# Optimization experiments

Measured on AMD Instinct MI355X. Metric: run time of the kernel, lower is better.

Reference implementation:

```python
import jax, jax.numpy as jnp
import numpy as np

B, L, D, H, E, K = 16, 197, 768, 12, 8, 2
HID = 4 * D
HD = D // H
SCALE = HD ** -0.5
EPS = 1e-5


def _layernorm(x, g, b):
    m = jnp.mean(x, axis=-1, keepdims=True)
    v = jnp.mean((x - m) ** 2, axis=-1, keepdims=True)
    return (x - m) * jax.lax.rsqrt(v + EPS) * g + b


def setup_inputs() -> dict:
    key = jax.random.key(0)
    ks = jax.random.split(key, 8)
    s = 0.02
    return {
        "x": jax.random.normal(ks[0], (B, L, D), jnp.float32),
        "ln1_g": jnp.ones((D,), jnp.float32),
        "ln1_b": jnp.zeros((D,), jnp.float32),
        "qkv_w": jax.random.normal(ks[1], (D, 3 * D), jnp.float32) * s,
        "qkv_b": jnp.zeros((3 * D,), jnp.float32),
        "proj_w": jax.random.normal(ks[2], (D, D), jnp.float32) * s,
        "proj_b": jnp.zeros((D,), jnp.float32),
        "ln2_g": jnp.ones((D,), jnp.float32),
        "ln2_b": jnp.zeros((D,), jnp.float32),
        "w_gate": jax.random.normal(ks[3], (D, E), jnp.float32) * s,
        "w1": jax.random.normal(ks[4], (E, D, HID), jnp.float32) * s,
        "b1": jnp.zeros((E, HID), jnp.float32),
        "w2": jax.random.normal(ks[5], (E, HID, D), jnp.float32) * s,
        "b2": jnp.zeros((E, D), jnp.float32),
    }


def reference(x, ln1_g, ln1_b, qkv_w, qkv_b, proj_w, proj_b,
              ln2_g, ln2_b, w_gate, w1, b1, w2, b2):
    # --- attention branch: x = x + attn(norm1(x)) ---
    h = _layernorm(x, ln1_g, ln1_b)
    qkv = (h @ qkv_w + qkv_b).reshape(B, L, 3, H, HD)
    q, k, v = [qkv[:, :, i].transpose(0, 2, 1, 3) for i in range(3)]  # [B,H,L,HD]
    attn = jax.nn.softmax(jnp.einsum('bhqd,bhkd->bhqk', q, k) * SCALE, axis=-1)
    o = jnp.einsum('bhqk,bhkd->bhqd', attn, v).transpose(0, 2, 1, 3).reshape(B, L, D)
    x = x + o @ proj_w + proj_b

    # --- MoE FFN branch on norm2(x), tokens flattened ---
    flat = _layernorm(x, ln2_g, ln2_b).reshape(-1, D)  # [T, D], T = B*L
    T = flat.shape[0]
    # noisy top-k gating, eval path (no noise): top-(k+1) logits, softmax over top-k
    logits = flat @ w_gate                              # [T, E]
    top_vals, top_idx = jax.lax.top_k(logits, K + 1)
    probs = jax.nn.softmax(top_vals[:, :K], axis=-1)    # [T, K]
    gates = jnp.zeros((T, E), flat.dtype).at[
        jnp.arange(T)[:, None], top_idx[:, :K]].set(probs)  # sparse gate matrix

    # dense equivalent of SparseDispatcher dispatch -> expert MLP -> combine:
    # output[t] = sum_e gates[t,e] * (gelu(flat @ w1[e] + b1[e]) @ w2[e] + b2[e])
    hid = jax.nn.gelu(jnp.einsum('td,edf->tef', flat, w1) + b1, approximate=False)
    y = jnp.einsum('te,tef,efd->td', gates, hid, w2) + gates @ b2
    return x + y.reshape(B, L, D)
```

## Files before the change

### kernel.cpp

```cpp
#include <hip/hip_runtime.h>
#include <math.h>
#include <stdint.h>

typedef unsigned short u16;
typedef unsigned int u32;
typedef float floatx4 __attribute__((ext_vector_type(4)));
typedef __bf16 bf16x8 __attribute__((ext_vector_type(8)));

#define T_TOK 3152
#define SEQ 197
#define NH 12
#define LISTN 7424
#define MOE_MT 58
#define YHALF ((size_t)LISTN * 768)

__device__ __forceinline__ float bf2f(u16 u) { return __uint_as_float(((u32)u) << 16); }
__device__ __forceinline__ u16 f2bf(float f) {
    u32 u = __float_as_uint(f);
    u += 0x7FFFu + ((u >> 16) & 1u);
    return (u16)(u >> 16);
}
__device__ __forceinline__ float wred_sum(float v) {
#pragma unroll
    for (int off = 32; off; off >>= 1) v += __shfl_xor(v, off);
    return v;
}

__device__ __forceinline__ float gelu_fast(float v) {
    float x = fabsf(v) * 0.70710678118654752f;
    float t = __builtin_amdgcn_rcpf(fmaf(0.3275911f, x, 1.0f));
    float p = t * fmaf(t, fmaf(t, fmaf(t, fmaf(t, 1.061405429f, -1.453152027f),
                                       1.421413741f), -0.284496736f), 0.254829592f);
    float er = fmaf(-p, __expf(-x * x), 1.0f);
    er = copysignf(er, v);
    return 0.5f * v * (1.0f + er);
}

#define GLB_AS(p) ((const __attribute__((address_space(1))) void*)(uintptr_t)(p))
#define LDS_AS(p) ((__attribute__((address_space(3))) void*)(uintptr_t)(p))
__device__ __forceinline__ void gl_lds16(const u16* g, u16* l) {
    __builtin_amdgcn_global_load_lds(GLB_AS(g), LDS_AS(l), 16, 0, 0);
}

template <int SPLIT>
__global__ __launch_bounds__(256) void transp_kernel(const float* __restrict__ in,
        u16* __restrict__ oh, u16* __restrict__ ol, int R, int C) {
    int r0 = blockIdx.x * 64, c0 = blockIdx.y * 64;
    size_t zo = (size_t)blockIdx.z * R * C;
    __shared__ float Lt[64][68];
    int tid = threadIdx.x;
    int rr = tid >> 2, cs = (tid & 3) * 16;
    const float* src = in + zo + (size_t)(r0 + rr) * C + c0 + cs;
#pragma unroll
    for (int i = 0; i < 4; i++) *(float4*)&Lt[rr][cs + i * 4] = *(const float4*)(src + i * 4);
    __syncthreads();
    int cw = tid >> 2, rs = (tid & 3) * 16;
    u16 hv[16], lv[16];
#pragma unroll
    for (int j = 0; j < 16; j++) {
        float v = Lt[rs + j][cw];
        u16 hb = f2bf(v);
        hv[j] = hb;
        if (SPLIT) lv[j] = f2bf(v - bf2f(hb));
    }
    u16* dst = oh + zo + (size_t)(c0 + cw) * R + r0 + rs;
    *(uint4*)dst = *(const uint4*)&hv[0];
    *(uint4*)(dst + 8) = *(const uint4*)&hv[8];
    if (SPLIT) {
        u16* dstl = ol + zo + (size_t)(c0 + cw) * R + r0 + rs;
        *(uint4*)dstl = *(const uint4*)&lv[0];
        *(uint4*)(dstl + 8) = *(const uint4*)&lv[8];
    }
}

__global__ __launch_bounds__(256) void ln1_kernel(const float* __restrict__ x,
        const float* __restrict__ g, const float* __restrict__ b,
        u16* __restrict__ h_hi, u16* __restrict__ h_lo) {
    int t = blockIdx.x, tid = threadIdx.x;
    int w = tid >> 6, lane = tid & 63;
    float v[3];
#pragma unroll
    for (int i = 0; i < 3; i++) v[i] = x[(size_t)t * 768 + tid + i * 256];
    float s = v[0] + v[1] + v[2];
    float q = v[0] * v[0] + v[1] * v[1] + v[2] * v[2];
    s = wred_sum(s); q = wred_sum(q);
    __shared__ float red[8];
    if (lane == 0) { red[w] = s; red[4 + w] = q; }
    __syncthreads();
    float st = red[0] + red[1] + red[2] + red[3];
    float qt = red[4] + red[5] + red[6] + red[7];
    float mean = st * (1.f / 768.f);
    float var = qt * (1.f / 768.f) - mean * mean;
    float rs = rsqrtf(var + 1e-5f);
#pragma unroll
    for (int i = 0; i < 3; i++) {
        int d = tid + i * 256;
        float hv = (v[i] - mean) * rs * g[d] + b[d];
        u16 hi = f2bf(hv);
        h_hi[(size_t)t * 768 + d] = hi;
        h_lo[(size_t)t * 768 + d] = f2bf(hv - bf2f(hi));
    }
}

template <int MODE>
__global__ __launch_bounds__(256) void gemm128(const u16* __restrict__ Ah,
        const u16* __restrict__ Al, const u16* __restrict__ Bh, const u16* __restrict__ Bl,
        const float* __restrict__ bias, void* __restrict__ Cv, void* __restrict__ Cv2,
        const float* __restrict__ resid,
        const int* __restrict__ list, const int* __restrict__ asg, int M, int N, int K) {
    constexpr bool SPLIT = (MODE <= 1);
    constexpr int GX = (MODE <= 1) ? 25 : MOE_MT;
    constexpr int GY = (MODE == 0) ? 18 : (MODE == 2) ? 24 : 6;
    constexpr int GZ = (MODE == 3) ? 2 : 1;
    constexpr int G  = GX * GY * GZ;
    constexpr int NT = GY * GZ;
    constexpr int Q8 = G >> 3, R8 = G & 7;

    int d = blockIdx.x + GX * (blockIdx.y + GY * blockIdx.z);
    int j = d & 7, s = d >> 3;
    int v = (j < R8) ? (j * (Q8 + 1) + s) : (R8 * (Q8 + 1) + (j - R8) * Q8 + s);
    int mt = v / NT, nzr = v - mt * NT;
    int yt = nzr % GY, zt = nzr / GY;
    int m0 = mt * 128, n0 = yt * 128;

    const u16* Bph = Bh;
    const float* bp = bias;
    const u16* Bpl = Bl;
    if (MODE >= 2) {
        if (m0 >= asg[8]) return;
        int e = 0;
        while (m0 >= asg[e + 1]) ++e;
        Bph = Bh + (size_t)e * N * K;
        bp = bias + (size_t)e * N;
    }
    int kbeg = 0, kend = K;
    if (MODE == 3) { int kh = K >> 1; kbeg = zt * kh; kend = kbeg + kh; }

    __shared__ __align__(16) u16 SM[32768];
    u16* Ash = SM;
    u16* Bsh = SM + (SPLIT ? 8192 : 16384);
    u16* Asl = SM + 16384;
    u16* Bsl = SM + 24576;

    int tid = threadIdx.x;
    int w = tid >> 6, lane = tid & 63, l15 = lane & 15, quad = lane >> 4;
    int wm = (w & 1) * 64, wn = (w >> 1) * 64;
    int lr = lane >> 2;
    int lc = ((lane & 3) ^ ((lane >> 3) & 3)) * 8;

    const u16* ga[2]; const u16* gal[2];
    const u16* gb[2]; const u16* gbl[2];
    int ldro[2];
#pragma unroll
    for (int it = 0; it < 2; it++) {
        int arow = m0 + it * 64 + w * 16 + lr;
        if (MODE == 2) {
            int entry = list[arow];
            ga[it] = Ah + (size_t)(entry >= 0 ? (entry >> 1) : 0) * K + lc;
        } else if (MODE == 3) {
            ga[it] = Ah + (size_t)arow * K + lc;
        } else {
            int rc = min(arow, M - 1);
            ga[it] = Ah + (size_t)rc * K + lc;
            gal[it] = Al + (size_t)rc * K + lc;
        }
        int brow = n0 + it * 64 + w * 16 + lr;
        gb[it] = Bph + (size_t)brow * K + lc;
        if (SPLIT) gbl[it] = Bpl + (size_t)brow * K + lc;
        ldro[it] = (it * 64 + w * 16) * 32;
    }

    int ra[4], rb[4];
#pragma unroll
    for (int i = 0; i < 4; i++) {
        int r1 = wm + i * 16 + l15;
        ra[i] = r1 * 32 + (quad ^ ((r1 >> 1) & 3)) * 8;
        int r2 = wn + i * 16 + l15;
        rb[i] = r2 * 32 + (quad ^ ((r2 >> 1) & 3)) * 8;
    }

    floatx4 acc[4][4];
#pragma unroll
    for (int mi = 0; mi < 4; mi++)
#pragma unroll
        for (int ni = 0; ni < 4; ni++) acc[mi][ni] = (floatx4){0.f, 0.f, 0.f, 0.f};

    auto stage = [&](int buf, int k0) {
        int bo = buf * 4096;
#pragma unroll
        for (int it = 0; it < 2; it++) {
            gl_lds16(ga[it] + k0, &Ash[bo + ldro[it]]);
            gl_lds16(gb[it] + k0, &Bsh[bo + ldro[it]]);
            if constexpr (SPLIT) {
                gl_lds16(gal[it] + k0, &Asl[bo + ldro[it]]);
                gl_lds16(gbl[it] + k0, &Bsl[bo + ldro[it]]);
            }
        }
    };
    auto compute = [&](int buf) {
        int bo = buf * 4096;
        bf16x8 afh[4], bfh[4], afl[4], bfl[4];
#pragma unroll
        for (int i = 0; i < 4; i++) {
            afh[i] = *(const bf16x8*)&Ash[bo + ra[i]];
            bfh[i] = *(const bf16x8*)&Bsh[bo + rb[i]];
            if constexpr (SPLIT) {
                afl[i] = *(const bf16x8*)&Asl[bo + ra[i]];
                bfl[i] = *(const bf16x8*)&Bsl[bo + rb[i]];
            }
        }
        if constexpr (!SPLIT) __builtin_amdgcn_s_setprio(1);
#pragma unroll
        for (int mi = 0; mi < 4; mi++)
#pragma unroll
            for (int ni = 0; ni < 4; ni++) {
                if constexpr (SPLIT) {
                    acc[mi][ni] = __builtin_amdgcn_mfma_f32_16x16x32_bf16(afl[mi], bfh[ni], acc[mi][ni], 0, 0, 0);
                    acc[mi][ni] = __builtin_amdgcn_mfma_f32_16x16x32_bf16(afh[mi], bfl[ni], acc[mi][ni], 0, 0, 0);
                }
                acc[mi][ni] = __builtin_amdgcn_mfma_f32_16x16x32_bf16(afh[mi], bfh[ni], acc[mi][ni], 0, 0, 0);
            }
        if constexpr (!SPLIT) __builtin_amdgcn_s_setprio(0);
    };

    int nsteps = (kend - kbeg) >> 5;
    if constexpr (SPLIT) {
        stage(0, kbeg);
        __syncthreads();
        for (int s2 = 0; s2 < nsteps; s2 += 2) {
            int k0 = kbeg + s2 * 32;
            stage(1, k0 + 32);
            compute(0);
            __syncthreads();
            if (s2 + 2 < nsteps) stage(0, k0 + 64);
            compute(1);
            __syncthreads();
        }
    } else {
        stage(0, kbeg);
        stage(1, kbeg + 32);
        stage(2, kbeg + 64);
        asm volatile("s_waitcnt vmcnt(8)" ::: "memory");
        __builtin_amdgcn_s_barrier();
        for (int t = 0; t < nsteps; ++t) {
            if (t + 3 < nsteps) stage((t + 3) & 3, kbeg + (t + 3) * 32);
            compute(t & 3);
            if (t + 3 < nsteps) {
                asm volatile("s_waitcnt vmcnt(8) lgkmcnt(0)" ::: "memory");
            } else if (t + 2 < nsteps) {
                asm volatile("s_waitcnt vmcnt(4) lgkmcnt(0)" ::: "memory");
            } else {
                asm volatile("s_waitcnt vmcnt(0) lgkmcnt(0)" ::: "memory");
            }
            __builtin_amdgcn_s_barrier();
        }
    }

    if constexpr (MODE == 2) {
#pragma unroll
        for (int ni = 0; ni < 4; ni++) {
            int col = wn + ni * 16 + l15;
            float bb = bp[n0 + col];
#pragma unroll
            for (int mi = 0; mi < 4; mi++) {
#pragma unroll
                for (int r = 0; r < 4; r++) {
                    int row = wm + mi * 16 + quad * 4 + r;
                    float gv = gelu_fast(acc[mi][ni][r] + bb);
                    SM[row * 128 + (col ^ ((row & 7) << 3))] = f2bf(gv);
                }
            }
        }
        __syncthreads();
        int rr = tid >> 1, half = (tid & 1) * 64;
        int grow = m0 + rr;
        if (list[grow] >= 0) {
            u16* dst = (u16*)Cv + (size_t)grow * N + n0 + half;
            int xr = (rr & 7) << 3;
#pragma unroll
            for (int gch = 0; gch < 8; gch++) {
                int cb = (half + gch * 8) ^ xr;
                *(uint4*)(dst + gch * 8) = *(const uint4*)&SM[rr * 128 + cb];
            }
        }
        return;
    }

    float* Cf = (float*)Cv;
    if (MODE == 3) Cf += (size_t)zt * ((size_t)M * N);
#pragma unroll
    for (int ni = 0; ni < 4; ni++) {
        int col = n0 + wn + ni * 16 + l15;
        float bb = bp[col];
        if (MODE == 3 && zt != 0) bb = 0.f;
#pragma unroll
        for (int mi = 0; mi < 4; mi++) {
#pragma unroll
            for (int r = 0; r < 4; r++) {
                int row = m0 + wm + mi * 16 + quad * 4 + r;
                float v2 = acc[mi][ni][r] + bb;
                if (MODE == 0) {
                    if (row < M) {
                        u16 hb = f2bf(v2);
                        ((u16*)Cv)[(size_t)row * N + col] = hb;
                        ((u16*)Cv2)[(size_t)row * N + col] = f2bf(v2 - bf2f(hb));
                    }
                } else if (MODE == 1) {
                    if (row < M) Cf[(size_t)row * N + col] = v2 + resid[(size_t)row * N + col];
                } else {
                    if (list[row] >= 0) Cf[(size_t)row * N + col] = v2;
                }
            }
        }
    }
}

__global__ __launch_bounds__(256) void attn_mfma_kernel(const u16* __restrict__ qph,
        const u16* __restrict__ qpl, u16* __restrict__ ohi, u16* __restrict__ olo) {
    int d = blockIdx.x + 4 * blockIdx.y;
    int j = d & 7, sdx = d >> 3;
    int v = j * 96 + sdx;
    int qbase = (v & 3) * 64;
    int by = v >> 2;
    int b = by / NH, h = by % NH;
    int tid = threadIdx.x;
    int w = tid >> 6, lane = tid & 63, l15 = lane & 15, quad = lane >> 4;

    __shared__ u16 Qh[64 * 64], Ql[64 * 64];
    __shared__ u16 Sh[64 * 64], Sl[64 * 64];
    __shared__ u16 Ph[64 * 72], Pl[64 * 72];

    int grow8 = lane >> 3;
    int gsrc = ((lane & 7) ^ grow8) * 8;
    int srow = tid >> 2;
    int scol = (tid & 3) * 16;

#pragma unroll
    for (int it = 0; it < 2; it++) {
        int r = qbase + w * 16 + it * 8 + grow8;
        int rc = min(r, SEQ - 1);
        size_t so = (size_t)(b * SEQ + rc) * 2304 + h * 64 + gsrc;
        gl_lds16(qph + so, &Qh[(w * 16 + it * 8) * 64]);
        gl_lds16(qpl + so, &Ql[(w * 16 + it * 8) * 64]);
    }
    __syncthreads();
    bf16x8 aqh[2], aql[2];
#pragma unroll
    for (int s2 = 0; s2 < 2; s2++) {
        int row = w * 16 + l15;
        int ad = row * 64 + (((s2 * 4 + quad) ^ (row & 7))) * 8;
        aqh[s2] = *(const bf16x8*)&Qh[ad];
        aql[s2] = *(const bf16x8*)&Ql[ad];
    }

    floatx4 sc[16];
#pragma unroll
    for (int f = 0; f < 16; f++) sc[f] = (floatx4){0.f, 0.f, 0.f, 0.f};

    for (int t = 0; t < 4; t++) {
#pragma unroll
        for (int it = 0; it < 2; it++) {
            int r = t * 64 + w * 16 + it * 8 + grow8;
            int rc = min(r, SEQ - 1);
            size_t so = (size_t)(b * SEQ + rc) * 2304 + 768 + h * 64 + gsrc;
            gl_lds16(qph + so, &Sh[(w * 16 + it * 8) * 64]);
            gl_lds16(qpl + so, &Sl[(w * 16 + it * 8) * 64]);
        }
        __syncthreads();
#pragma unroll
        for (int s = 0; s < 4; s++) {
            int row = s * 16 + l15;
#pragma unroll
            for (int s2 = 0; s2 < 2; s2++) {
                int ad = row * 64 + (((s2 * 4 + quad) ^ (row & 7))) * 8;
                bf16x8 bkh = *(const bf16x8*)&Sh[ad];
                bf16x8 bkl = *(const bf16x8*)&Sl[ad];
                sc[t * 4 + s] = __builtin_amdgcn_mfma_f32_16x16x32_bf16(aql[s2], bkh, sc[t * 4 + s], 0, 0, 0);
                sc[t * 4 + s] = __builtin_amdgcn_mfma_f32_16x16x32_bf16(aqh[s2], bkl, sc[t * 4 + s], 0, 0, 0);
                sc[t * 4 + s] = __builtin_amdgcn_mfma_f32_16x16x32_bf16(aqh[s2], bkh, sc[t * 4 + s], 0, 0, 0);
            }
        }
        __syncthreads();
    }

    float m[4] = {-1e30f, -1e30f, -1e30f, -1e30f};
#pragma unroll
    for (int f = 0; f < 16; f++) {
        int key = (f >> 2) * 64 + (f & 3) * 16 + l15;
        bool valid = key < SEQ;
#pragma unroll
        for (int r = 0; r < 4; r++) {
            float s = valid ? sc[f][r] * 0.125f : -1e30f;
            sc[f][r] = s;
            m[r] = fmaxf(m[r], s);
        }
    }
#pragma unroll
    for (int r = 0; r < 4; r++) {
#pragma unroll
        for (int off = 1; off < 16; off <<= 1) m[r] = fmaxf(m[r], __shfl_xor(m[r], off));
    }
    float sum[4] = {0.f, 0.f, 0.f, 0.f};
#pragma unroll
    for (int f = 0; f < 16; f++) {
#pragma unroll
        for (int r = 0; r < 4; r++) {
            float p = expf(sc[f][r] - m[r]);
            sc[f][r] = p;
            sum[r] += p;
        }
    }
    float inv[4];
#pragma unroll
    for (int r = 0; r < 4; r++) {
#pragma unroll
        for (int off = 1; off < 16; off <<= 1) sum[r] += __shfl_xor(sum[r], off);
        inv[r] = 1.f / sum[r];
    }

    floatx4 oacc[4];
#pragma unroll
    for (int sd = 0; sd < 4; sd++) oacc[sd] = (floatx4){0.f, 0.f, 0.f, 0.f};

    for (int t = 0; t < 4; t++) {
#pragma unroll
        for (int s = 0; s < 4; s++) {
#pragma unroll
            for (int r = 0; r < 4; r++) {
                float p = sc[t * 4 + s][r];
                u16 hb = f2bf(p);
                int row = w * 16 + quad * 4 + r;
                Ph[row * 72 + s * 16 + l15] = hb;
                Pl[row * 72 + s * 16 + l15] = f2bf(p - bf2f(hb));
            }
        }
        {
            int key = t * 64 + srow;
            int kc = min(key, SEQ - 1);
            size_t so = (size_t)(b * SEQ + kc) * 2304 + 1536 + h * 64 + scol;
            u16 hv[16], lv[16];
            *(uint4*)&hv[0] = *(const uint4*)(qph + so);
            *(uint4*)&hv[8] = *(const uint4*)(qph + so + 8);
            *(uint4*)&lv[0] = *(const uint4*)(qpl + so);
            *(uint4*)&lv[8] = *(const uint4*)(qpl + so + 8);
            int kg = srow >> 3, kw = srow & 7;
#pragma unroll
            for (int i = 0; i < 16; i++) {
                int dcol = scol + i;
                int idx = dcol * 64 + ((kg ^ (dcol & 7)) * 8) + kw;
                Sh[idx] = hv[i];
                Sl[idx] = lv[i];
            }
        }
        __syncthreads();
#pragma unroll
        for (int s2 = 0; s2 < 2; s2++) {
            bf16x8 aph = *(const bf16x8*)&Ph[(w * 16 + l15) * 72 + s2 * 32 + quad * 8];
            bf16x8 apl = *(const bf16x8*)&Pl[(w * 16 + l15) * 72 + s2 * 32 + quad * 8];
#pragma unroll
            for (int sd = 0; sd < 4; sd++) {
                int row = sd * 16 + l15;
                int ad = row * 64 + (((s2 * 4 + quad) ^ (row & 7))) * 8;
                bf16x8 bvh = *(const bf16x8*)&Sh[ad];
                bf16x8 bvl = *(const bf16x8*)&Sl[ad];
                oacc[sd] = __builtin_amdgcn_mfma_f32_16x16x32_bf16(apl, bvh, oacc[sd], 0, 0, 0);
                oacc[sd] = __builtin_amdgcn_mfma_f32_16x16x32_bf16(aph, bvl, oacc[sd], 0, 0, 0);
                oacc[sd] = __builtin_amdgcn_mfma_f32_16x16x32_bf16(aph, bvh, oacc[sd], 0, 0, 0);
            }
        }
        __syncthreads();
    }

#pragma unroll
    for (int sd = 0; sd < 4; sd++) {
#pragma unroll
        for (int r = 0; r < 4; r++) {
            int q = qbase + w * 16 + quad * 4 + r;
            if (q < SEQ) {
                float val = oacc[sd][r] * inv[r];
                u16 hb = f2bf(val);
                size_t o = ((size_t)(b * SEQ + q)) * 768 + h * 64 + sd * 16 + l15;
                ohi[o] = hb;
                olo[o] = f2bf(val - bf2f(hb));
            }
        }
    }
}

__global__ __launch_bounds__(256) void ln2_gate_kernel(const float* __restrict__ x1,
        const float* __restrict__ g, const float* __restrict__ b, const float* __restrict__ wg,
        u16* __restrict__ flat, int2* __restrict__ idx, float2* __restrict__ gate) {
    int t = blockIdx.x, tid = threadIdx.x;
    int w = tid >> 6, lane = tid & 63;
    float v[3];
#pragma unroll
    for (int i = 0; i < 3; i++) v[i] = x1[(size_t)t * 768 + tid + i * 256];
    float s = v[0] + v[1] + v[2];
    float q = v[0] * v[0] + v[1] * v[1] + v[2] * v[2];
    s = wred_sum(s); q = wred_sum(q);
    __shared__ float red[8];
    __shared__ float fs[768];
    __shared__ float lg[8];
    if (lane == 0) { red[w] = s; red[4 + w] = q; }
    __syncthreads();
    float st = red[0] + red[1] + red[2] + red[3];
    float qt = red[4] + red[5] + red[6] + red[7];
    float mean = st * (1.f / 768.f);
    float var = qt * (1.f / 768.f) - mean * mean;
    float rs = rsqrtf(var + 1e-5f);
#pragma unroll
    for (int i = 0; i < 3; i++) {
        int d = tid + i * 256;
        float f = (v[i] - mean) * rs * g[d] + b[d];
        flat[(size_t)t * 768 + d] = f2bf(f);
        fs[d] = f;
    }
    __syncthreads();
    int e0 = 2 * w, e1 = 2 * w + 1;
    float p0 = 0.f, p1 = 0.f;
    for (int d = lane; d < 768; d += 64) {
        float f = fs[d];
        p0 += f * wg[d * 8 + e0];
        p1 += f * wg[d * 8 + e1];
    }
    p0 = wred_sum(p0); p1 = wred_sum(p1);
    if (lane == 0) { lg[e0] = p0; lg[e1] = p1; }
    __syncthreads();
    if (tid == 0) {
        float b0 = -1e30f, b1 = -1e30f;
        int i0 = 0, i1 = 0;
        for (int e = 0; e < 8; e++) {
            float le = lg[e];
            if (le > b0) { b1 = b0; i1 = i0; b0 = le; i0 = e; }
            else if (le > b1) { b1 = le; i1 = e; }
        }
        float ex = expf(b1 - b0);
        float den = 1.f + ex;
        idx[t] = make_int2(i0, i1);
        gate[t] = make_float2(1.f / den, ex / den);
    }
}

__global__ __launch_bounds__(256) void hist_kernel(const int2* __restrict__ idx, int* __restrict__ cnt) {
    int t = blockIdx.x * 256 + threadIdx.x;
    if (t < T_TOK) {
        int2 id = idx[t];
        atomicAdd(&cnt[id.x], 1);
        atomicAdd(&cnt[id.y], 1);
    }
}

__global__ void offsets_kernel(const int* __restrict__ cnt, int* __restrict__ asg) {
    if (threadIdx.x == 0 && blockIdx.x == 0) {
        int acc = 0;
        asg[0] = 0;
        for (int e = 0; e < 8; e++) { acc += (cnt[e] + 127) & ~127; asg[e + 1] = acc; }
    }
}

__global__ __launch_bounds__(256) void scatter_kernel(const int2* __restrict__ idx,
        const int* __restrict__ asg, int* __restrict__ cursor,
        int* __restrict__ list, int* __restrict__ pos) {
    int t = blockIdx.x * 256 + threadIdx.x;
    if (t >= T_TOK) return;
    int2 id = idx[t];
    int p0 = asg[id.x] + atomicAdd(&cursor[id.x], 1);
    list[p0] = t * 2;
    pos[t * 2] = p0;
    int p1 = asg[id.y] + atomicAdd(&cursor[id.y], 1);
    list[p1] = t * 2 + 1;
    pos[t * 2 + 1] = p1;
}

__global__ __launch_bounds__(256) void final_kernel(const float* __restrict__ x1,
        const float* __restrict__ yp, const int* __restrict__ pos,
        const float2* __restrict__ gate, float* __restrict__ out) {
    int t = blockIdx.x, tid = threadIdx.x;
    float2 g = gate[t];
    int p0 = pos[t * 2], p1 = pos[t * 2 + 1];
#pragma unroll
    for (int i = 0; i < 3; i++) {
        int d = tid + i * 256;
        float y0 = yp[(size_t)p0 * 768 + d] + yp[YHALF + (size_t)p0 * 768 + d];
        float y1 = yp[(size_t)p1 * 768 + d] + yp[YHALF + (size_t)p1 * 768 + d];
        out[(size_t)t * 768 + d] = x1[(size_t)t * 768 + d] + g.x * y0 + g.y * y1;
    }
}

extern "C" void kernel_launch(void* const* d_in, const int* in_sizes, int n_in,
                              void* d_out, int out_size, void* d_ws, size_t ws_size,
                              hipStream_t stream) {
    const float* x      = (const float*)d_in[0];
    const float* ln1_g  = (const float*)d_in[1];
    const float* ln1_b  = (const float*)d_in[2];
    const float* qkv_w  = (const float*)d_in[3];
    const float* qkv_b  = (const float*)d_in[4];
    const float* proj_w = (const float*)d_in[5];
    const float* proj_b = (const float*)d_in[6];
    const float* ln2_g  = (const float*)d_in[7];
    const float* ln2_b  = (const float*)d_in[8];
    const float* w_gate = (const float*)d_in[9];
    const float* w1     = (const float*)d_in[10];
    const float* b1     = (const float*)d_in[11];
    const float* w2     = (const float*)d_in[12];
    const float* b2     = (const float*)d_in[13];

    char* ws = (char*)d_ws;
    size_t off = 0;
    auto alloc = [&](size_t bytes) { size_t cur = off; off = (off + bytes + 255) & ~(size_t)255; return cur; };
    u16*    h_hi   = (u16*)   (ws + alloc((size_t)T_TOK * 768 * 2));
    u16*    h_lo   = (u16*)   (ws + alloc((size_t)T_TOK * 768 * 2));
    u16*    qkv_hi = (u16*)   (ws + alloc((size_t)T_TOK * 2304 * 2));
    u16*    qkv_lo = (u16*)   (ws + alloc((size_t)T_TOK * 2304 * 2));
    u16*    o_hi   = (u16*)   (ws + alloc((size_t)T_TOK * 768 * 2));
    u16*    o_lo   = (u16*)   (ws + alloc((size_t)T_TOK * 768 * 2));
    float*  ypair  = (float*) ws;
    float*  x1     = (float*) (ws + alloc((size_t)T_TOK * 768 * 4));
    u16*    flat   = (u16*)   (ws + alloc((size_t)T_TOK * 768 * 2));
    int2*   idx    = (int2*)  (ws + alloc((size_t)T_TOK * 8));
    float2* gate   = (float2*)(ws + alloc((size_t)T_TOK * 8));
    int*    cnt    = (int*)   (ws + alloc(64));
    int*    cursor = cnt + 8;
    int*    asg    = (int*)   (ws + alloc(64));
    int*    list   = (int*)   (ws + alloc((size_t)LISTN * 4));
    int*    pos    = (int*)   (ws + alloc((size_t)T_TOK * 2 * 4));
    u16*    hid    = (u16*)   (ws + alloc((size_t)LISTN * 3072 * 2));
    u16*    qkvt_h = (u16*)   (ws + alloc((size_t)2304 * 768 * 2));
    u16*    qkvt_l = (u16*)   (ws + alloc((size_t)2304 * 768 * 2));
    u16*    projt_h = (u16*)  (ws + alloc((size_t)768 * 768 * 2));
    u16*    projt_l = (u16*)  (ws + alloc((size_t)768 * 768 * 2));
    u16*    w1t    = (u16*)   (ws + alloc((size_t)8 * 3072 * 768 * 2));
    u16*    w2t    = (u16*)   (ws + alloc((size_t)8 * 768 * 3072 * 2));

    hipMemsetAsync(cnt, 0, 64, stream);
    hipMemsetAsync(list, 0xFF, (size_t)LISTN * 4, stream);

    transp_kernel<1><<<dim3(12, 36, 1), 256, 0, stream>>>(qkv_w, qkvt_h, qkvt_l, 768, 2304);
    transp_kernel<1><<<dim3(12, 12, 1), 256, 0, stream>>>(proj_w, projt_h, projt_l, 768, 768);
    transp_kernel<0><<<dim3(12, 48, 8), 256, 0, stream>>>(w1, w1t, nullptr, 768, 3072);
    transp_kernel<0><<<dim3(48, 12, 8), 256, 0, stream>>>(w2, w2t, nullptr, 3072, 768);

    ln1_kernel<<<T_TOK, 256, 0, stream>>>(x, ln1_g, ln1_b, h_hi, h_lo);
    gemm128<0><<<dim3(25, 18), 256, 0, stream>>>(h_hi, h_lo, qkvt_h, qkvt_l, qkv_b, qkv_hi,
                                                 qkv_lo, nullptr, nullptr, nullptr, T_TOK, 2304, 768);
    attn_mfma_kernel<<<dim3(4, 192), 256, 0, stream>>>(qkv_hi, qkv_lo, o_hi, o_lo);
    gemm128<1><<<dim3(25, 6), 256, 0, stream>>>(o_hi, o_lo, projt_h, projt_l, proj_b, x1,
                                                nullptr, x, nullptr, nullptr, T_TOK, 768, 768);
    ln2_gate_kernel<<<T_TOK, 256, 0, stream>>>(x1, ln2_g, ln2_b, w_gate, flat, idx, gate);
    hist_kernel<<<(T_TOK + 255) / 256, 256, 0, stream>>>(idx, cnt);
    offsets_kernel<<<1, 64, 0, stream>>>(cnt, asg);
    scatter_kernel<<<(T_TOK + 255) / 256, 256, 0, stream>>>(idx, asg, cursor, list, pos);
    gemm128<2><<<dim3(MOE_MT, 24), 256, 0, stream>>>(flat, nullptr, w1t, nullptr, b1, hid,
                                                     nullptr, nullptr, list, asg, LISTN, 3072, 768);
    gemm128<3><<<dim3(MOE_MT, 6, 2), 256, 0, stream>>>(hid, nullptr, w2t, nullptr, b2, ypair,
                                                       nullptr, nullptr, list, asg, LISTN, 768, 3072);
    final_kernel<<<T_TOK, 256, 0, stream>>>(x1, ypair, pos, gate, (float*)d_out);
}
```

Before: 536.8 us.

## Use a 256x256-tile 512-thread kernel for the MoE first GEMM

Replaces the 128x128 MODE-2 expert up-projection GEMM with a dedicated 256x256-tile kernel. It runs eight waves, double-buffers LDS and fuses gathered-row loads with the bias+GELU epilogue. The goal is more data reuse per loaded tile and fewer weight re-reads. To match the tile, expert segments are padded to 256 rows, which enlarges the list and adds some padding work. The down-projection GEMM drops from a 4-stage to a 3-stage LDS pipeline to cut shared memory, and its second split-K partial is written into the dead w1t buffer.

Measured after the change: 653.9 us. +21.8%, slower.

```diff
diff --git a/kernel.cpp b/kernel.cpp
--- a/kernel.cpp
+++ b/kernel.cpp
@@ -10,9 +10,9 @@
 #define T_TOK 3152
 #define SEQ 197
 #define NH 12
-#define LISTN 7424
-#define MOE_MT 58
-#define YHALF ((size_t)LISTN * 768)
+#define LISTN 8448
+#define MOE1_MT 33
+#define MOE2_MT 66
 
 __device__ __forceinline__ float bf2f(u16 u) { return __uint_as_float(((u32)u) << 16); }
 __device__ __forceinline__ u16 f2bf(float f) {
@@ -109,8 +109,8 @@
         const float* __restrict__ resid,
         const int* __restrict__ list, const int* __restrict__ asg, int M, int N, int K) {
     constexpr bool SPLIT = (MODE <= 1);
-    constexpr int GX = (MODE <= 1) ? 25 : MOE_MT;
-    constexpr int GY = (MODE == 0) ? 18 : (MODE == 2) ? 24 : 6;
+    constexpr int GX = (MODE <= 1) ? 25 : MOE2_MT;
+    constexpr int GY = (MODE == 0) ? 18 : 6;
     constexpr int GZ = (MODE == 3) ? 2 : 1;
     constexpr int G  = GX * GY * GZ;
     constexpr int NT = GY * GZ;
@@ -126,7 +126,7 @@
     const u16* Bph = Bh;
     const float* bp = bias;
     const u16* Bpl = Bl;
-    if (MODE >= 2) {
+    if (MODE == 3) {
         if (m0 >= asg[8]) return;
         int e = 0;
         while (m0 >= asg[e + 1]) ++e;
@@ -136,9 +136,9 @@
     int kbeg = 0, kend = K;
     if (MODE == 3) { int kh = K >> 1; kbeg = zt * kh; kend = kbeg + kh; }
 
-    __shared__ __align__(16) u16 SM[32768];
+    __shared__ __align__(16) u16 SM[SPLIT ? 32768 : 24576];
     u16* Ash = SM;
-    u16* Bsh = SM + (SPLIT ? 8192 : 16384);
+    u16* Bsh = SM + (SPLIT ? 8192 : 12288);
     u16* Asl = SM + 16384;
     u16* Bsl = SM + 24576;
 
@@ -154,10 +154,7 @@
 #pragma unroll
     for (int it = 0; it < 2; it++) {
         int arow = m0 + it * 64 + w * 16 + lr;
-        if (MODE == 2) {
-            int entry = list[arow];
-            ga[it] = Ah + (size_t)(entry >= 0 ? (entry >> 1) : 0) * K + lc;
-        } else if (MODE == 3) {
+        if (MODE == 3) {
             ga[it] = Ah + (size_t)arow * K + lc;
         } else {
             int rc = min(arow, M - 1);
@@ -239,55 +236,25 @@
     } else {
         stage(0, kbeg);
         stage(1, kbeg + 32);
-        stage(2, kbeg + 64);
-        asm volatile("s_waitcnt vmcnt(8)" ::: "memory");
+        asm volatile("s_waitcnt vmcnt(4)" ::: "memory");
         __builtin_amdgcn_s_barrier();
+        int bufc = 0;
         for (int t = 0; t < nsteps; ++t) {
-            if (t + 3 < nsteps) stage((t + 3) & 3, kbeg + (t + 3) * 32);
-            compute(t & 3);
-            if (t + 3 < nsteps) {
-                asm volatile("s_waitcnt vmcnt(8) lgkmcnt(0)" ::: "memory");
-            } else if (t + 2 < nsteps) {
+            int b2 = bufc + 2; if (b2 >= 3) b2 -= 3;
+            if (t + 2 < nsteps) stage(b2, kbeg + (t + 2) * 32);
+            compute(bufc);
+            if (t + 2 < nsteps) {
                 asm volatile("s_waitcnt vmcnt(4) lgkmcnt(0)" ::: "memory");
             } else {
                 asm volatile("s_waitcnt vmcnt(0) lgkmcnt(0)" ::: "memory");
             }
             __builtin_amdgcn_s_barrier();
-        }
-    }
-
-    if constexpr (MODE == 2) {
-#pragma unroll
-        for (int ni = 0; ni < 4; ni++) {
-            int col = wn + ni * 16 + l15;
-            float bb = bp[n0 + col];
-#pragma unroll
-            for (int mi = 0; mi < 4; mi++) {
-#pragma unroll
-                for (int r = 0; r < 4; r++) {
-                    int row = wm + mi * 16 + quad * 4 + r;
-                    float gv = gelu_fast(acc[mi][ni][r] + bb);
-                    SM[row * 128 + (col ^ ((row & 7) << 3))] = f2bf(gv);
-                }
-            }
-        }
-        __syncthreads();
-        int rr = tid >> 1, half = (tid & 1) * 64;
-        int grow = m0 + rr;
-        if (list[grow] >= 0) {
-            u16* dst = (u16*)Cv + (size_t)grow * N + n0 + half;
-            int xr = (rr & 7) << 3;
-#pragma unroll
-            for (int gch = 0; gch < 8; gch++) {
-                int cb = (half + gch * 8) ^ xr;
-                *(uint4*)(dst + gch * 8) = *(const uint4*)&SM[rr * 128 + cb];
-            }
-        }
-        return;
+            bufc = (bufc == 2) ? 0 : bufc + 1;
+        }
     }
 
     float* Cf = (float*)Cv;
-    if (MODE == 3) Cf += (size_t)zt * ((size_t)M * N);
+    if (MODE == 3 && zt != 0) Cf = (float*)Cv2;
 #pragma unroll
     for (int ni = 0; ni < 4; ni++) {
         int col = n0 + wn + ni * 16 + l15;
@@ -315,6 +282,122 @@
     }
 }
 
+__global__ __launch_bounds__(512, 1) void gemm256_moe1(const u16* __restrict__ Ah,
+        const u16* __restrict__ Bh, const float* __restrict__ bias, u16* __restrict__ Cv,
+        const int* __restrict__ list, const int* __restrict__ asg) {
+    constexpr int GX = MOE1_MT, GY = 12, G = GX * GY;
+    constexpr int Q8 = G >> 3, R8 = G & 7;
+    constexpr int N = 3072, K = 768, NSTEP = 24;
+
+    int d = blockIdx.x + GX * blockIdx.y;
+    int j = d & 7, s = d >> 3;
+    int v = (j < R8) ? (j * (Q8 + 1) + s) : (R8 * (Q8 + 1) + (j - R8) * Q8 + s);
+    int mt = v / GY, yt = v - mt * GY;
+    int m0 = mt * 256, n0 = yt * 256;
+    if (m0 >= asg[8]) return;
+    int e = 0;
+    while (m0 >= asg[e + 1]) ++e;
+    const u16* Bph = Bh + (size_t)e * N * K;
+    const float* bp = bias + (size_t)e * N;
+
+    __shared__ __align__(16) u16 SM[32768];
+
+    int tid = threadIdx.x;
+    int w = tid >> 6, lane = tid & 63, l15 = lane & 15, quad = lane >> 4;
+    int wr = w >> 2, wc = w & 3;
+    int lc = ((lane & 3) ^ ((lane >> 3) & 3)) * 8;
+
+    int ar0 = m0 + (tid >> 2);
+    int le0 = list[ar0], le1 = list[ar0 + 128];
+    const u16* gA0 = Ah + (size_t)(le0 >= 0 ? (le0 >> 1) : 0) * K + lc;
+    const u16* gA1 = Ah + (size_t)(le1 >= 0 ? (le1 >> 1) : 0) * K + lc;
+    const u16* gB0 = Bph + (size_t)(n0 + (tid >> 2)) * K + lc;
+    const u16* gB1 = Bph + (size_t)(n0 + 128 + (tid >> 2)) * K + lc;
+    int chunk = w * 512;
+
+    int ra[8], rb[4];
+#pragma unroll
+    for (int i = 0; i < 8; i++) { int r = wr * 128 + i * 16 + l15; ra[i] = r * 32 + (quad ^ ((r >> 1) & 3)) * 8; }
+#pragma unroll
+    for (int i = 0; i < 4; i++) { int r = wc * 64 + i * 16 + l15; rb[i] = r * 32 + (quad ^ ((r >> 1) & 3)) * 8; }
+
+    floatx4 acc[8][4];
+#pragma unroll
+    for (int i = 0; i < 8; i++)
+#pragma unroll
+        for (int j2 = 0; j2 < 4; j2++) acc[i][j2] = (floatx4){0.f, 0.f, 0.f, 0.f};
+
+    auto stage = [&](int buf, int k0) {
+        u16* la = &SM[buf * 8192];
+        u16* lb = &SM[16384 + buf * 8192];
+        gl_lds16(gA0 + k0, la + chunk);
+        gl_lds16(gA1 + k0, la + 4096 + chunk);
+        gl_lds16(gB0 + k0, lb + chunk);
+        gl_lds16(gB1 + k0, lb + 4096 + chunk);
+    };
+    auto compute = [&](int buf) {
+        const u16* la = &SM[buf * 8192];
+        const u16* lb = &SM[16384 + buf * 8192];
+        bf16x8 af[8], bf[4];
+#pragma unroll
+        for (int i = 0; i < 8; i++) af[i] = *(const bf16x8*)&la[ra[i]];
+#pragma unroll
+        for (int i = 0; i < 4; i++) bf[i] = *(const bf16x8*)&lb[rb[i]];
+        __builtin_amdgcn_s_setprio(1);
+#pragma unroll
+        for (int i = 0; i < 8; i++)
+#pragma unroll
+            for (int j2 = 0; j2 < 4; j2++)
+                acc[i][j2] = __builtin_amdgcn_mfma_f32_16x16x32_bf16(af[i], bf[j2], acc[i][j2], 0, 0, 0);
+        __builtin_amdgcn_s_setprio(0);
+    };
+
+    stage(0, 0);
+    for (int t = 0; t < NSTEP; ++t) {
+        if (t + 1 < NSTEP) {
+            stage((t + 1) & 1, (t + 1) * 32);
+            asm volatile("s_waitcnt vmcnt(4)" ::: "memory");
+        } else {
+            asm volatile("s_waitcnt vmcnt(0)" ::: "memory");
+        }
+        __builtin_amdgcn_s_barrier();
+        compute(t & 1);
+        __builtin_amdgcn_s_barrier();
+    }
+
+#pragma unroll
+    for (int p = 0; p < 2; p++) {
+        if (wr == p) {
+#pragma unroll
+            for (int j2 = 0; j2 < 4; j2++) {
+                int col = wc * 64 + j2 * 16 + l15;
+                float bb = bp[n0 + col];
+#pragma unroll
+                for (int i = 0; i < 8; i++) {
+#pragma unroll
+                    for (int r = 0; r < 4; r++) {
+                        int row = i * 16 + quad * 4 + r;
+                        SM[row * 256 + (col ^ ((row & 7) << 3))] = f2bf(gelu_fast(acc[i][j2][r] + bb));
+                    }
+                }
+            }
+        }
+        __syncthreads();
+        int row = tid >> 2, cb0 = (tid & 3) * 64;
+        int grow = m0 + p * 128 + row;
+        if (list[grow] >= 0) {
+            u16* dst = Cv + (size_t)grow * N + n0 + cb0;
+            int xr = (row & 7) << 3;
+#pragma unroll
+            for (int ch = 0; ch < 8; ch++) {
+                int cc = (cb0 + ch * 8) ^ xr;
+                *(uint4*)(dst + ch * 8) = *(const uint4*)&SM[row * 256 + cc];
+            }
+        }
+        __syncthreads();
+    }
+}
+
 __global__ __launch_bounds__(256) void attn_mfma_kernel(const u16* __restrict__ qph,
         const u16* __restrict__ qpl, u16* __restrict__ ohi, u16* __restrict__ olo) {
     int d = blockIdx.x + 4 * blockIdx.y;
@@ -554,7 +637,7 @@
     if (threadIdx.x == 0 && blockIdx.x == 0) {
         int acc = 0;
         asg[0] = 0;
-        for (int e = 0; e < 8; e++) { acc += (cnt[e] + 127) & ~127; asg[e + 1] = acc; }
+        for (int e = 0; e < 8; e++) { acc += (cnt[e] + 255) & ~255; asg[e + 1] = acc; }
     }
 }
 
@@ -573,7 +656,7 @@
 }
 
 __global__ __launch_bounds__(256) void final_kernel(const float* __restrict__ x1,
-        const float* __restrict__ yp, const int* __restrict__ pos,
+        const float* __restrict__ yp0, const float* __restrict__ yp1, const int* __restrict__ pos,
         const float2* __restrict__ gate, float* __restrict__ out) {
     int t = blockIdx.x, tid = threadIdx.x;
     float2 g = gate[t];
@@ -581,8 +664,8 @@
 #pragma unroll
     for (int i = 0; i < 3; i++) {
         int d = tid + i * 256;
-        float y0 = yp[(size_t)p0 * 768 + d] + yp[YHALF + (size_t)p0 * 768 + d];
-        float y1 = yp[(size_t)p1 * 768 + d] + yp[YHALF + (size_t)p1 * 768 + d];
+        float y0 = yp0[(size_t)p0 * 768 + d] + yp1[(size_t)p0 * 768 + d];
+        float y1 = yp0[(size_t)p1 * 768 + d] + yp1[(size_t)p1 * 768 + d];
         out[(size_t)t * 768 + d] = x1[(size_t)t * 768 + d] + g.x * y0 + g.y * y1;
     }
 }
@@ -614,7 +697,7 @@
     u16*    qkv_lo = (u16*)   (ws + alloc((size_t)T_TOK * 2304 * 2));
     u16*    o_hi   = (u16*)   (ws + alloc((size_t)T_TOK * 768 * 2));
     u16*    o_lo   = (u16*)   (ws + alloc((size_t)T_TOK * 768 * 2));
-    float*  ypair  = (float*) ws;
+    float*  ypair0 = (float*) ws;
     float*  x1     = (float*) (ws + alloc((size_t)T_TOK * 768 * 4));
     u16*    flat   = (u16*)   (ws + alloc((size_t)T_TOK * 768 * 2));
     int2*   idx    = (int2*)  (ws + alloc((size_t)T_TOK * 8));
@@ -631,6 +714,7 @@
     u16*    projt_l = (u16*)  (ws + alloc((size_t)768 * 768 * 2));
     u16*    w1t    = (u16*)   (ws + alloc((size_t)8 * 3072 * 768 * 2));
     u16*    w2t    = (u16*)   (ws + alloc((size_t)8 * 768 * 3072 * 2));
+    float*  ypair1 = (float*) w1t;
 
     hipMemsetAsync(cnt, 0, 64, stream);
     hipMemsetAsync(list, 0xFF, (size_t)LISTN * 4, stream);
@@ -650,9 +734,8 @@
     hist_kernel<<<(T_TOK + 255) / 256, 256, 0, stream>>>(idx, cnt);
     offsets_kernel<<<1, 64, 0, stream>>>(cnt, asg);
     scatter_kernel<<<(T_TOK + 255) / 256, 256, 0, stream>>>(idx, asg, cursor, list, pos);
-    gemm128<2><<<dim3(MOE_MT, 24), 256, 0, stream>>>(flat, nullptr, w1t, nullptr, b1, hid,
-                                                     nullptr, nullptr, list, asg, LISTN, 3072, 768);
-    gemm128<3><<<dim3(MOE_MT, 6, 2), 256, 0, stream>>>(hid, nullptr, w2t, nullptr, b2, ypair,
-                                                       nullptr, nullptr, list, asg, LISTN, 768, 3072);
-    final_kernel<<<T_TOK, 256, 0, stream>>>(x1, ypair, pos, gate, (float*)d_out);
-}
+    gemm256_moe1<<<dim3(MOE1_MT, 12), 512, 0, stream>>>(flat, w1t, b1, hid, list, asg);
+    gemm128<3><<<dim3(MOE2_MT, 6, 2), 256, 0, stream>>>(hid, nullptr, w2t, nullptr, b2, ypair0,
+                                                        ypair1, nullptr, list, asg, LISTN, 768, 3072);
+    final_kernel<<<T_TOK, 256, 0, stream>>>(x1, ypair0, ypair1, pos, gate, (float*)d_out);
+}
```

## Rework GEMM LDS pipelining and fuse expert histogram into gating kernel

Applied to the files above, without the earlier changes.

The SPLIT GEMM path switches from a double buffer with full __syncthreads to explicit vmcnt waits and raw barriers, and it now raises wave priority around the MFMA block. The non-split path goes from four to three LDS stages, which shrinks shared memory to allow more resident blocks at the cost of a shallower prefetch. The expert-count histogram moves into ln2_gate_kernel as atomics, removing one kernel launch. The second split-K partial buffer is relocated into the w1t region, which is dead by the time the second expert GEMM runs.

Result: slower. 583.7 us (+8.7%).

```diff
diff --git a/kernel.cpp b/kernel.cpp
--- a/kernel.cpp
+++ b/kernel.cpp
@@ -12,7 +12,6 @@
 #define NH 12
 #define LISTN 7424
 #define MOE_MT 58
-#define YHALF ((size_t)LISTN * 768)
 
 __device__ __forceinline__ float bf2f(u16 u) { return __uint_as_float(((u32)u) << 16); }
 __device__ __forceinline__ u16 f2bf(float f) {
@@ -136,9 +135,9 @@
     int kbeg = 0, kend = K;
     if (MODE == 3) { int kh = K >> 1; kbeg = zt * kh; kend = kbeg + kh; }
 
-    __shared__ __align__(16) u16 SM[32768];
+    __shared__ __align__(16) u16 SM[SPLIT ? 32768 : 24576];
     u16* Ash = SM;
-    u16* Bsh = SM + (SPLIT ? 8192 : 16384);
+    u16* Bsh = SM + (SPLIT ? 8192 : 12288);
     u16* Asl = SM + 16384;
     u16* Bsl = SM + 24576;
 
@@ -209,7 +208,7 @@
                 bfl[i] = *(const bf16x8*)&Bsl[bo + rb[i]];
             }
         }
-        if constexpr (!SPLIT) __builtin_amdgcn_s_setprio(1);
+        __builtin_amdgcn_s_setprio(1);
 #pragma unroll
         for (int mi = 0; mi < 4; mi++)
 #pragma unroll
@@ -220,39 +219,43 @@
                 }
                 acc[mi][ni] = __builtin_amdgcn_mfma_f32_16x16x32_bf16(afh[mi], bfh[ni], acc[mi][ni], 0, 0, 0);
             }
-        if constexpr (!SPLIT) __builtin_amdgcn_s_setprio(0);
+        __builtin_amdgcn_s_setprio(0);
     };
 
     int nsteps = (kend - kbeg) >> 5;
     if constexpr (SPLIT) {
         stage(0, kbeg);
-        __syncthreads();
-        for (int s2 = 0; s2 < nsteps; s2 += 2) {
-            int k0 = kbeg + s2 * 32;
-            stage(1, k0 + 32);
-            compute(0);
-            __syncthreads();
-            if (s2 + 2 < nsteps) stage(0, k0 + 64);
-            compute(1);
-            __syncthreads();
+        stage(1, kbeg + 32);
+        asm volatile("s_waitcnt vmcnt(8)" ::: "memory");
+        __builtin_amdgcn_s_barrier();
+        for (int t = 0; t < nsteps; ++t) {
+            compute(t & 1);
+            asm volatile("s_waitcnt lgkmcnt(0)" ::: "memory");
+            __builtin_amdgcn_s_barrier();
+            if (t + 2 < nsteps) {
+                stage(t & 1, kbeg + (t + 2) * 32);
+                asm volatile("s_waitcnt vmcnt(8)" ::: "memory");
+            } else if (t + 1 < nsteps) {
+                asm volatile("s_waitcnt vmcnt(0)" ::: "memory");
+            }
         }
     } else {
         stage(0, kbeg);
         stage(1, kbeg + 32);
-        stage(2, kbeg + 64);
-        asm volatile("s_waitcnt vmcnt(8)" ::: "memory");
+        asm volatile("s_waitcnt vmcnt(4)" ::: "memory");
         __builtin_amdgcn_s_barrier();
+        int bufc = 0;
         for (int t = 0; t < nsteps; ++t) {
-            if (t + 3 < nsteps) stage((t + 3) & 3, kbeg + (t + 3) * 32);
-            compute(t & 3);
-            if (t + 3 < nsteps) {
-                asm volatile("s_waitcnt vmcnt(8) lgkmcnt(0)" ::: "memory");
-            } else if (t + 2 < nsteps) {
+            int b2 = bufc + 2; if (b2 >= 3) b2 -= 3;
+            if (t + 2 < nsteps) stage(b2, kbeg + (t + 2) * 32);
+            compute(bufc);
+            if (t + 2 < nsteps) {
                 asm volatile("s_waitcnt vmcnt(4) lgkmcnt(0)" ::: "memory");
             } else {
                 asm volatile("s_waitcnt vmcnt(0) lgkmcnt(0)" ::: "memory");
             }
             __builtin_amdgcn_s_barrier();
+            bufc = (bufc == 2) ? 0 : bufc + 1;
         }
     }
 
@@ -287,7 +290,7 @@
     }
 
     float* Cf = (float*)Cv;
-    if (MODE == 3) Cf += (size_t)zt * ((size_t)M * N);
+    if (MODE == 3 && zt != 0) Cf = (float*)Cv2;
 #pragma unroll
     for (int ni = 0; ni < 4; ni++) {
         int col = n0 + wn + ni * 16 + l15;
@@ -489,7 +492,8 @@
 
 __global__ __launch_bounds__(256) void ln2_gate_kernel(const float* __restrict__ x1,
         const float* __restrict__ g, const float* __restrict__ b, const float* __restrict__ wg,
-        u16* __restrict__ flat, int2* __restrict__ idx, float2* __restrict__ gate) {
+        u16* __restrict__ flat, int2* __restrict__ idx, float2* __restrict__ gate,
+        int* __restrict__ cnt) {
     int t = blockIdx.x, tid = threadIdx.x;
     int w = tid >> 6, lane = tid & 63;
     float v[3];
@@ -538,15 +542,8 @@
         float den = 1.f + ex;
         idx[t] = make_int2(i0, i1);
         gate[t] = make_float2(1.f / den, ex / den);
-    }
-}
-
-__global__ __launch_bounds__(256) void hist_kernel(const int2* __restrict__ idx, int* __restrict__ cnt) {
-    int t = blockIdx.x * 256 + threadIdx.x;
-    if (t < T_TOK) {
-        int2 id = idx[t];
-        atomicAdd(&cnt[id.x], 1);
-        atomicAdd(&cnt[id.y], 1);
+        atomicAdd(&cnt[i0], 1);
+        atomicAdd(&cnt[i1], 1);
     }
 }
 
@@ -573,7 +570,7 @@
 }
 
 __global__ __launch_bounds__(256) void final_kernel(const float* __restrict__ x1,
-        const float* __restrict__ yp, const int* __restrict__ pos,
+        const float* __restrict__ yp0, const float* __restrict__ yp1, const int* __restrict__ pos,
         const float2* __restrict__ gate, float* __restrict__ out) {
     int t = blockIdx.x, tid = threadIdx.x;
     float2 g = gate[t];
@@ -581,8 +578,8 @@
 #pragma unroll
     for (int i = 0; i < 3; i++) {
         int d = tid + i * 256;
-        float y0 = yp[(size_t)p0 * 768 + d] + yp[YHALF + (size_t)p0 * 768 + d];
-        float y1 = yp[(size_t)p1 * 768 + d] + yp[YHALF + (size_t)p1 * 768 + d];
+        float y0 = yp0[(size_t)p0 * 768 + d] + yp1[(size_t)p0 * 768 + d];
+        float y1 = yp0[(size_t)p1 * 768 + d] + yp1[(size_t)p1 * 768 + d];
         out[(size_t)t * 768 + d] = x1[(size_t)t * 768 + d] + g.x * y0 + g.y * y1;
     }
 }
@@ -614,7 +611,7 @@
     u16*    qkv_lo = (u16*)   (ws + alloc((size_t)T_TOK * 2304 * 2));
     u16*    o_hi   = (u16*)   (ws + alloc((size_t)T_TOK * 768 * 2));
     u16*    o_lo   = (u16*)   (ws + alloc((size_t)T_TOK * 768 * 2));
-    float*  ypair  = (float*) ws;
+    float*  ypair0 = (float*) ws;
     float*  x1     = (float*) (ws + alloc((size_t)T_TOK * 768 * 4));
     u16*    flat   = (u16*)   (ws + alloc((size_t)T_TOK * 768 * 2));
     int2*   idx    = (int2*)  (ws + alloc((size_t)T_TOK * 8));
@@ -631,6 +628,7 @@
     u16*    projt_l = (u16*)  (ws + alloc((size_t)768 * 768 * 2));
     u16*    w1t    = (u16*)   (ws + alloc((size_t)8 * 3072 * 768 * 2));
     u16*    w2t    = (u16*)   (ws + alloc((size_t)8 * 768 * 3072 * 2));
+    float*  ypair1 = (float*) w1t;
 
     hipMemsetAsync(cnt, 0, 64, stream);
     hipMemsetAsync(list, 0xFF, (size_t)LISTN * 4, stream);
@@ -646,13 +644,12 @@
     attn_mfma_kernel<<<dim3(4, 192), 256, 0, stream>>>(qkv_hi, qkv_lo, o_hi, o_lo);
     gemm128<1><<<dim3(25, 6), 256, 0, stream>>>(o_hi, o_lo, projt_h, projt_l, proj_b, x1,
                                                 nullptr, x, nullptr, nullptr, T_TOK, 768, 768);
-    ln2_gate_kernel<<<T_TOK, 256, 0, stream>>>(x1, ln2_g, ln2_b, w_gate, flat, idx, gate);
-    hist_kernel<<<(T_TOK + 255) / 256, 256, 0, stream>>>(idx, cnt);
+    ln2_gate_kernel<<<T_TOK, 256, 0, stream>>>(x1, ln2_g, ln2_b, w_gate, flat, idx, gate, cnt);
     offsets_kernel<<<1, 64, 0, stream>>>(cnt, asg);
     scatter_kernel<<<(T_TOK + 255) / 256, 256, 0, stream>>>(idx, asg, cursor, list, pos);
     gemm128<2><<<dim3(MOE_MT, 24), 256, 0, stream>>>(flat, nullptr, w1t, nullptr, b1, hid,
                                                      nullptr, nullptr, list, asg, LISTN, 3072, 768);
-    gemm128<3><<<dim3(MOE_MT, 6, 2), 256, 0, stream>>>(hid, nullptr, w2t, nullptr, b2, ypair,
-                                                       nullptr, nullptr, list, asg, LISTN, 768, 3072);
-    final_kernel<<<T_TOK, 256, 0, stream>>>(x1, ypair, pos, gate, (float*)d_out);
-}
+    gemm128<3><<<dim3(MOE_MT, 6, 2), 256, 0, stream>>>(hid, nullptr, w2t, nullptr, b2, ypair0,
+                                                       ypair1, nullptr, list, asg, LISTN, 768, 3072);
+    final_kernel<<<T_TOK, 256, 0, stream>>>(x1, ypair0, ypair1, pos, gate, (float*)d_out);
+}
```
